# Optimization experiments

Measured on AMD Instinct MI355X. Metric: run time of the kernel, lower is better.

Reference implementation:

```python
import jax, jax.numpy as jnp
import numpy as np

BIG = 1e8   # fill value used by to_dense_batch for missing neighbors in the original
EPS_W = 1e-8
EPS_BN = 1e-5


def setup_inputs() -> dict:
    key = jax.random.key(0)
    ks = jax.random.split(key, 8)
    N, S, Dc, Df = 16384, 4096, 256, 64
    fine_xyz = jax.random.normal(ks[0], (1, 3, N), dtype=jnp.float32)
    coarse_xyz = jax.random.normal(ks[1], (1, 3, S), dtype=jnp.float32)
    fine_piece_id = jnp.sort(jax.random.randint(ks[2], (1, 1, N), 0, 4))
    coarse_piece_id = jnp.sort(jax.random.randint(ks[3], (1, 1, S), 0, 4))
    fine_features = jax.random.normal(ks[4], (1, Df, N), dtype=jnp.float32)
    coarse_features = jax.random.normal(ks[5], (1, Dc, S), dtype=jnp.float32)
    # mlp stack: Conv1d(320->256), Conv1d(256->128), each with BatchNorm1d
    W1 = jax.random.normal(ks[6], (256, Dc + Df), dtype=jnp.float32) * 0.05
    b1 = jnp.zeros((256,), jnp.float32)
    g1 = jnp.ones((256,), jnp.float32)
    be1 = jnp.zeros((256,), jnp.float32)
    W2 = jax.random.normal(ks[7], (128, 256), dtype=jnp.float32) * 0.05
    b2 = jnp.zeros((128,), jnp.float32)
    g2 = jnp.ones((128,), jnp.float32)
    be2 = jnp.zeros((128,), jnp.float32)
    return dict(fine_xyz=fine_xyz, coarse_xyz=coarse_xyz,
                fine_piece_id=fine_piece_id, coarse_piece_id=coarse_piece_id,
                fine_features=fine_features, coarse_features=coarse_features,
                W1=W1, b1=b1, g1=g1, be1=be1, W2=W2, b2=b2, g2=g2, be2=be2)


def _bn_relu(x, gamma, beta):
    # x: [N, C]; BatchNorm1d in training mode -> batch stats over the N axis
    mu = jnp.mean(x, axis=0, keepdims=True)
    var = jnp.mean((x - mu) ** 2, axis=0, keepdims=True)  # biased var, as torch BN
    return jax.nn.relu((x - mu) * jax.lax.rsqrt(var + EPS_BN) * gamma + beta)


def reference(fine_xyz, coarse_xyz, fine_piece_id, coarse_piece_id,
              fine_features, coarse_features, W1, b1, g1, be1, W2, b2, g2, be2):
    fxyz = fine_xyz[0].T            # [N, 3]
    cxyz = coarse_xyz[0].T          # [S, 3]
    ff = fine_features[0].T         # [N, Df]
    cf = coarse_features[0].T       # [S, Dc]
    fid = fine_piece_id.reshape(-1)     # [N]
    cid = coarse_piece_id.reshape(-1)   # [S]

    # squared euclidean distances, masked to the same piece (knn with batch vectors)
    d2 = (jnp.sum(fxyz ** 2, -1)[:, None] + jnp.sum(cxyz ** 2, -1)[None, :]
          - 2.0 * fxyz @ cxyz.T)                       # [N, S]
    d2 = jnp.where(fid[:, None] != cid[None, :], BIG, d2)

    neg_d, idx = jax.lax.top_k(-d2, 3)                  # 3-NN per fine point
    dist = -neg_d                                       # [N, 3]

    w = 1.0 / (dist + EPS_W)
    w = w / jnp.sum(w, axis=1, keepdims=True)           # [N, 3]

    gathered = cf[idx]                                  # [N, 3, Dc]
    interp = jnp.sum(gathered * w[:, :, None], axis=1)  # [N, Dc]

    x = jnp.concatenate([interp, ff], axis=-1)          # [N, Dc+Df]
    x = _bn_relu(x @ W1.T + b1, g1, be1)                # [N, 256]
    x = _bn_relu(x @ W2.T + b2, g2, be2)                # [N, 128]
    return x.T[None]                                    # [1, 128, N]
```

## Files before the change

kernel.cpp:

```cpp
#include <hip/hip_runtime.h>
#include <hip/hip_bf16.h>

#define N_FINE   16384
#define S_COARSE 4096
#define DC       256
#define DF       64
#define K1       320
#define C1       256
#define C2       128
#define BIGF     1e8f
#define EPS_W    1e-8f
#define EPS_BN   1e-5f
#define IMAX     0x7fffffff

typedef __attribute__((ext_vector_type(8))) short bf16x8;
typedef __attribute__((ext_vector_type(8))) unsigned short u16x8;
typedef __attribute__((ext_vector_type(4))) float f32x4;

#define OFF_CNT    128
#define OFF_RANGES 0
#define OFF_SUMS   256
#define OFF_SCALE1 3328
#define OFF_SHIFT1 4352
#define OFF_SCALE2 5376
#define OFF_SHIFT2 5888
#define OFF_CPACK  8192
#define OFF_CFT    73728
#define OFF_IDX3   4268032
#define OFF_W3     4464640
#define OFF_W1B    4661248
#define OFF_W2B    4825088
#define OFF_Y1     4890624
#define OFF_Y2     13279232

__device__ inline unsigned short f2bf_bits(float f) {
    __hip_bfloat16 h = __float2bfloat16(f);
    unsigned short u;
    __builtin_memcpy(&u, &h, 2);
    return u;
}

__global__ __launch_bounds__(256) void setup_kernel(
    const int* __restrict__ cid, int* __restrict__ ranges, float* __restrict__ sums,
    int* __restrict__ cnt,
    const float* __restrict__ cxyz, float4* __restrict__ cpack,
    const float* __restrict__ W1, const float* __restrict__ W2,
    unsigned short* __restrict__ W1b, unsigned short* __restrict__ W2b,
    const float* __restrict__ cf, float* __restrict__ cfT)
{
    __shared__ float tile[32][33];
    int b = blockIdx.x, t = threadIdx.x;
    if (b == 0) {
        if (t < 8) ranges[t] = 0;
        if (t < 2) cnt[t] = 0;
        for (int i = t; i < 768; i += 256) sums[i] = 0.f;
        __syncthreads();
        for (int s = t; s < S_COARSE; s += 256) {
            int c = cid[s];
            if (s == 0 || cid[s - 1] != c) ranges[c] = s;
            if (s == S_COARSE - 1 || cid[s + 1] != c) ranges[4 + c] = s + 1;
        }
    } else if (b <= 16) {
        int s = (b - 1) * 256 + t;
        float x = cxyz[s], y = cxyz[S_COARSE + s], z = cxyz[2 * S_COARSE + s];
        cpack[s] = make_float4(x, y, z, x * x + y * y + z * z);
    } else if (b <= 336) {
        int i = (b - 17) * 256 + t;
        W1b[i] = f2bf_bits(W1[i]);
        if (i < C2 * C1) W2b[i] = f2bf_bits(W2[i]);
    } else {
        int lb = b - 337;
        int tx = t & 31, ty = t >> 5;
        int s0 = (lb & 127) * 32, c0 = (lb >> 7) * 32;
        #pragma unroll
        for (int i = 0; i < 4; i++)
            tile[ty + i * 8][tx] = cf[(c0 + ty + i * 8) * S_COARSE + s0 + tx];
        __syncthreads();
        #pragma unroll
        for (int i = 0; i < 4; i++) {
            int s = ty + i * 8;
            cfT[(s0 + s) * DC + c0 + tx] = tile[tx][s];
        }
    }
}

__global__ __launch_bounds__(256) void knn_kernel(const float* __restrict__ fxyz,
                                                  const int* __restrict__ fpid,
                                                  const float4* __restrict__ cpack,
                                                  const int* __restrict__ ranges,
                                                  int* __restrict__ idx3,
                                                  float* __restrict__ w3) {
    int t = threadIdx.x;
    int lane = t & 63, wid = t >> 6;
    int n = blockIdx.x * 4 + wid;
    int fid = fpid[n];
    float fx = fxyz[n], fy = fxyz[N_FINE + n], fz = fxyz[2 * N_FINE + n];
    float fn2 = fx * fx + fy * fy + fz * fz;
    int st = ranges[fid], en = ranges[4 + fid];

    float d0 = BIGF, d1 = BIGF, d2v = BIGF;
    int i0 = IMAX, i1 = IMAX, i2 = IMAX;
    for (int s = st + lane; s < en; s += 64) {
        float4 c = cpack[s];
        float d = fn2 + c.w - 2.0f * (fx * c.x + fy * c.y + fz * c.z);
        if (d < d0)       { d2v = d1; i2 = i1; d1 = d0; i1 = i0; d0 = d; i0 = s; }
        else if (d < d1)  { d2v = d1; i2 = i1; d1 = d;  i1 = s; }
        else if (d < d2v) { d2v = d;  i2 = s; }
    }
    #pragma unroll
    for (int m = 1; m < 64; m <<= 1) {
        float e0 = __shfl_xor(d0, m, 64), e1 = __shfl_xor(d1, m, 64), e2 = __shfl_xor(d2v, m, 64);
        int   j0 = __shfl_xor(i0, m, 64), j1 = __shfl_xor(i1, m, 64), j2 = __shfl_xor(i2, m, 64);
        #pragma unroll
        for (int q = 0; q < 3; q++) {
            float e = (q == 0) ? e0 : (q == 1) ? e1 : e2;
            int   j = (q == 0) ? j0 : (q == 1) ? j1 : j2;
            bool b0 = (e < d0) || (e == d0 && j < i0);
            bool b1 = (e < d1) || (e == d1 && j < i1);
            bool b2 = (e < d2v) || (e == d2v && j < i2);
            if (b0)      { d2v = d1; i2 = i1; d1 = d0; i1 = i0; d0 = e; i0 = j; }
            else if (b1) { d2v = d1; i2 = i1; d1 = e;  i1 = j; }
            else if (b2) { d2v = e;  i2 = j; }
        }
    }
    if (lane == 0) {
        int cand = 0;
        while (i0 == IMAX || i1 == IMAX || i2 == IMAX) {
            if (cand >= st && cand < en) { cand = en; continue; }
            if (i0 == IMAX)      { i0 = cand; d0 = BIGF; }
            else if (i1 == IMAX) { i1 = cand; d1 = BIGF; }
            else                 { i2 = cand; d2v = BIGF; }
            cand++;
        }
        float w0 = 1.0f / (d0 + EPS_W);
        float w1 = 1.0f / (d1 + EPS_W);
        float w2 = 1.0f / (d2v + EPS_W);
        float inv = 1.0f / (w0 + w1 + w2);
        idx3[n * 3 + 0] = i0; idx3[n * 3 + 1] = i1; idx3[n * 3 + 2] = i2;
        w3[n * 3 + 0] = w0 * inv; w3[n * 3 + 1] = w1 * inv; w3[n * 3 + 2] = w2 * inv;
    }
}

__global__ __launch_bounds__(256) void gemm1_kernel(
    const int* __restrict__ idx3, const float* __restrict__ w3,
    const float* __restrict__ cfT, const float* __restrict__ ff,
    const unsigned short* __restrict__ W1b, const float* __restrict__ bias,
    unsigned short* __restrict__ Y1, float* __restrict__ sums, float* __restrict__ sumsq,
    const float* __restrict__ g, const float* __restrict__ be,
    float* __restrict__ scale, float* __restrict__ shift, int* __restrict__ cnt)
{
    __shared__ __align__(16) unsigned short As[4 * 32 * 8];
    __shared__ __align__(16) unsigned short Bs[4 * 256 * 8];
    __shared__ int   sI[32][3];
    __shared__ float sWt[32][3];
    __shared__ int isLast;
    int t = threadIdx.x;
    int m0 = blockIdx.x * 32;
    int lane = t & 63, wid = t >> 6;
    int wn = wid * 64;

    if (t < 32) {
        sI[t][0]  = idx3[(m0 + t) * 3 + 0];
        sI[t][1]  = idx3[(m0 + t) * 3 + 1];
        sI[t][2]  = idx3[(m0 + t) * 3 + 2];
        sWt[t][0] = w3[(m0 + t) * 3 + 0];
        sWt[t][1] = w3[(m0 + t) * 3 + 1];
        sWt[t][2] = w3[(m0 + t) * 3 + 2];
    }
    int ksA = t & 3, rowA = t >> 2;
    int fxw = ksA << 2;
    int gA = ksA * 32 + (rowA ^ fxw);
    int rowB = t;
    f32x4 acc[2][4] = {};
    int ks = lane >> 4, r16 = lane & 15, fxr = ks << 2;
    __syncthreads();

    for (int kt = 0; kt < K1; kt += 32) {
        u16x8 va;
        if (t < 128) {
            int k0 = kt + ksA * 8;
            if (k0 < DC) {
                int i0 = sI[rowA][0], i1 = sI[rowA][1], i2 = sI[rowA][2];
                float w0 = sWt[rowA][0], w1 = sWt[rowA][1], w2 = sWt[rowA][2];
                const float* c0p = &cfT[i0 * DC + k0];
                const float* c1p = &cfT[i1 * DC + k0];
                const float* c2p = &cfT[i2 * DC + k0];
                float4 a0 = *(const float4*)c0p, a1 = *(const float4*)(c0p + 4);
                float4 b0 = *(const float4*)c1p, b1 = *(const float4*)(c1p + 4);
                float4 e0 = *(const float4*)c2p, e1 = *(const float4*)(c2p + 4);
                va[0] = f2bf_bits(w0 * a0.x + w1 * b0.x + w2 * e0.x);
                va[1] = f2bf_bits(w0 * a0.y + w1 * b0.y + w2 * e0.y);
                va[2] = f2bf_bits(w0 * a0.z + w1 * b0.z + w2 * e0.z);
                va[3] = f2bf_bits(w0 * a0.w + w1 * b0.w + w2 * e0.w);
                va[4] = f2bf_bits(w0 * a1.x + w1 * b1.x + w2 * e1.x);
                va[5] = f2bf_bits(w0 * a1.y + w1 * b1.y + w2 * e1.y);
                va[6] = f2bf_bits(w0 * a1.z + w1 * b1.z + w2 * e1.z);
                va[7] = f2bf_bits(w0 * a1.w + w1 * b1.w + w2 * e1.w);
            } else {
                int c = k0 - DC;
                #pragma unroll
                for (int i = 0; i < 8; i++)
                    va[i] = f2bf_bits(ff[(c + i) * N_FINE + m0 + rowA]);
            }
        }
        u16x8 vb[4];
        #pragma unroll
        for (int kb = 0; kb < 4; kb++)
            vb[kb] = *(const u16x8*)&W1b[(size_t)rowB * K1 + kt + kb * 8];
        __syncthreads();
        if (t < 128) *(u16x8*)&As[gA * 8] = va;
        #pragma unroll
        for (int kb = 0; kb < 4; kb++)
            *(u16x8*)&Bs[(kb * 256 + (rowB ^ (kb << 2))) * 8] = vb[kb];
        __syncthreads();
        bf16x8 af[2], bfr[4];
        #pragma unroll
        for (int mi = 0; mi < 2; mi++)
            af[mi] = *(const bf16x8*)&As[(ks * 32 + ((mi * 16 + r16) ^ fxr)) * 8];
        #pragma unroll
        for (int nj = 0; nj < 4; nj++)
            bfr[nj] = *(const bf16x8*)&Bs[(ks * 256 + ((wn + nj * 16 + r16) ^ fxr)) * 8];
        #pragma unroll
        for (int mi = 0; mi < 2; mi++)
            #pragma unroll
            for (int nj = 0; nj < 4; nj++)
                acc[mi][nj] = __builtin_amdgcn_mfma_f32_16x16x32_bf16(af[mi], bfr[nj], acc[mi][nj], 0, 0, 0);
    }

    float sl[4] = {0.f, 0.f, 0.f, 0.f}, s2l[4] = {0.f, 0.f, 0.f, 0.f};
    #pragma unroll
    for (int nj = 0; nj < 4; nj++) {
        int n = wn + nj * 16 + r16;
        float bb = bias[n];
        #pragma unroll
        for (int mi = 0; mi < 2; mi++) {
            #pragma unroll
            for (int r = 0; r < 4; r++) {
                int m = m0 + mi * 16 + ks * 4 + r;
                float o = acc[mi][nj][r] + bb;
                Y1[(size_t)m * C1 + n] = f2bf_bits(o);
                sl[nj] += o; s2l[nj] += o * o;
            }
        }
    }
    #pragma unroll
    for (int nj = 0; nj < 4; nj++) {
        sl[nj]  += __shfl_xor(sl[nj],  16, 64);
        sl[nj]  += __shfl_xor(sl[nj],  32, 64);
        s2l[nj] += __shfl_xor(s2l[nj], 16, 64);
        s2l[nj] += __shfl_xor(s2l[nj], 32, 64);
    }
    if (lane < 16) {
        #pragma unroll
        for (int nj = 0; nj < 4; nj++) {
            atomicAdd(&sums[wn + nj * 16 + lane],  sl[nj]);
            atomicAdd(&sumsq[wn + nj * 16 + lane], s2l[nj]);
        }
    }
    __threadfence();
    __syncthreads();
    if (t == 0) isLast = (atomicAdd(cnt, 1) == (int)gridDim.x - 1);
    __syncthreads();
    if (isLast && t < C1) {
        float s  = atomicAdd(&sums[t], 0.f);
        float s2 = atomicAdd(&sumsq[t], 0.f);
        float mean = s * (1.0f / N_FINE);
        float var = s2 * (1.0f / N_FINE) - mean * mean;
        float sc = g[t] * rsqrtf(var + EPS_BN);
        scale[t] = sc;
        shift[t] = be[t] - mean * sc;
    }
}

template <int KDIM, int NOUT>
__global__ __launch_bounds__(256) void mfma_gemm2_kernel(
    const unsigned short* __restrict__ A,
    const unsigned short* __restrict__ B,
    const float* __restrict__ bias,
    const float* __restrict__ scale,
    const float* __restrict__ shift,
    float* __restrict__ Yout,
    float* __restrict__ sums, float* __restrict__ sumsq,
    const float* __restrict__ g, const float* __restrict__ be,
    float* __restrict__ scale2, float* __restrict__ shift2, int* __restrict__ cnt)
{
    __shared__ __align__(16) unsigned short As[4 * 128 * 8];
    __shared__ __align__(16) unsigned short Bs[4 * 64 * 8];
    __shared__ int isLast;
    int t = threadIdx.x;
    int m0 = blockIdx.x * 128, j0 = blockIdx.y * 64;
    int lane = t & 63, wid = t >> 6;
    int wm = (wid >> 1) * 64, wn = (wid & 1) * 32;

    int ksA = t & 3;
    int rowA0 = t >> 2;
    int rowA1 = 64 + rowA0;
    int fxw = ksA << 2;
    int gA0 = ksA * 128 + (rowA0 ^ fxw);
    int gA1 = ksA * 128 + (rowA1 ^ fxw);
    int gB  = ksA * 64 + (rowA0 ^ fxw);
    const unsigned short* pa0 = A + (size_t)(m0 + rowA0) * KDIM + ksA * 8;
    const unsigned short* pa1 = A + (size_t)(m0 + rowA1) * KDIM + ksA * 8;
    const unsigned short* pb  = B + (size_t)(j0 + rowA0) * KDIM + ksA * 8;

    f32x4 acc[4][2] = {};
    int ks = lane >> 4, r16 = lane & 15;
    int fxr = ks << 2;

    for (int kt = 0; kt < KDIM; kt += 32) {
        u16x8 va0 = *(const u16x8*)(pa0 + kt);
        u16x8 va1 = *(const u16x8*)(pa1 + kt);
        u16x8 vb  = *(const u16x8*)(pb + kt);
        int kb = kt + ksA * 8;
        #pragma unroll
        for (int i = 0; i < 8; i++) {
            float sc = scale[kb + i], sh = shift[kb + i];
            float f0 = __uint_as_float(((unsigned)va0[i]) << 16);
            float f1 = __uint_as_float(((unsigned)va1[i]) << 16);
            va0[i] = f2bf_bits(fmaxf(fmaf(f0, sc, sh), 0.f));
            va1[i] = f2bf_bits(fmaxf(fmaf(f1, sc, sh), 0.f));
        }
        __syncthreads();
        *(u16x8*)&As[gA0 * 8] = va0;
        *(u16x8*)&As[gA1 * 8] = va1;
        *(u16x8*)&Bs[gB * 8]  = vb;
        __syncthreads();
        bf16x8 af[4], bfr[2];
        #pragma unroll
        for (int mi = 0; mi < 4; mi++)
            af[mi] = *(const bf16x8*)&As[(ks * 128 + wm + mi * 16 + (r16 ^ fxr)) * 8];
        #pragma unroll
        for (int nj = 0; nj < 2; nj++)
            bfr[nj] = *(const bf16x8*)&Bs[(ks * 64 + wn + nj * 16 + (r16 ^ fxr)) * 8];
        #pragma unroll
        for (int mi = 0; mi < 4; mi++)
            #pragma unroll
            for (int nj = 0; nj < 2; nj++)
                acc[mi][nj] = __builtin_amdgcn_mfma_f32_16x16x32_bf16(af[mi], bfr[nj], acc[mi][nj], 0, 0, 0);
    }

    float sl[2] = {0.f, 0.f}, s2l[2] = {0.f, 0.f};
    #pragma unroll
    for (int nj = 0; nj < 2; nj++) {
        int n = j0 + wn + nj * 16 + r16;
        float bb = bias[n];
        #pragma unroll
        for (int mi = 0; mi < 4; mi++) {
            #pragma unroll
            for (int r = 0; r < 4; r++) {
                int m = m0 + wm + mi * 16 + ks * 4 + r;
                float o = acc[mi][nj][r] + bb;
                Yout[(size_t)m * NOUT + n] = o;
                sl[nj] += o; s2l[nj] += o * o;
            }
        }
    }
    #pragma unroll
    for (int nj = 0; nj < 2; nj++) {
        sl[nj]  += __shfl_xor(sl[nj],  16, 64);
        sl[nj]  += __shfl_xor(sl[nj],  32, 64);
        s2l[nj] += __shfl_xor(s2l[nj], 16, 64);
        s2l[nj] += __shfl_xor(s2l[nj], 32, 64);
    }
    if (lane < 16) {
        atomicAdd(&sums[j0 + wn + lane],       sl[0]);
        atomicAdd(&sums[j0 + wn + 16 + lane],  sl[1]);
        atomicAdd(&sumsq[j0 + wn + lane],      s2l[0]);
        atomicAdd(&sumsq[j0 + wn + 16 + lane], s2l[1]);
    }
    __threadfence();
    __syncthreads();
    if (t == 0) isLast = (atomicAdd(cnt, 1) == (int)(gridDim.x * gridDim.y) - 1);
    __syncthreads();
    if (isLast && t < NOUT) {
        float s  = atomicAdd(&sums[t], 0.f);
        float s2 = atomicAdd(&sumsq[t], 0.f);
        float mean = s * (1.0f / N_FINE);
        float var = s2 * (1.0f / N_FINE) - mean * mean;
        float sc = g[t] * rsqrtf(var + EPS_BN);
        scale2[t] = sc;
        shift2[t] = be[t] - mean * sc;
    }
}

__global__ __launch_bounds__(256) void out_kernel(const float* __restrict__ Y2,
                                                  const float* __restrict__ scale2,
                                                  const float* __restrict__ shift2,
                                                  float* __restrict__ out) {
    __shared__ float tile[64][65];
    int t = threadIdx.x;
    int n0 = blockIdx.x * 64, c0 = blockIdx.y * 64;
    int cl = t & 63, rg = t >> 6;
    #pragma unroll
    for (int i = 0; i < 16; i++) {
        int r = rg + i * 4;
        tile[r][cl] = Y2[(n0 + r) * C2 + c0 + cl];
    }
    __syncthreads();
    #pragma unroll
    for (int i = 0; i < 16; i++) {
        int c = rg + i * 4;
        float v = fmaf(tile[cl][c], scale2[c0 + c], shift2[c0 + c]);
        out[(c0 + c) * N_FINE + n0 + cl] = fmaxf(v, 0.f);
    }
}

extern "C" void kernel_launch(void* const* d_in, const int* in_sizes, int n_in,
                              void* d_out, int out_size, void* d_ws, size_t ws_size,
                              hipStream_t stream) {
    const float* fine_xyz   = (const float*)d_in[0];
    const float* coarse_xyz = (const float*)d_in[1];
    const int*   fine_pid   = (const int*)d_in[2];
    const int*   coarse_pid = (const int*)d_in[3];
    const float* fine_feat  = (const float*)d_in[4];
    const float* coarse_feat= (const float*)d_in[5];
    const float* W1  = (const float*)d_in[6];
    const float* b1  = (const float*)d_in[7];
    const float* g1  = (const float*)d_in[8];
    const float* be1 = (const float*)d_in[9];
    const float* W2  = (const float*)d_in[10];
    const float* b2  = (const float*)d_in[11];
    const float* g2  = (const float*)d_in[12];
    const float* be2 = (const float*)d_in[13];
    float* out = (float*)d_out;

    char* ws = (char*)d_ws;
    int*    ranges = (int*)(ws + OFF_RANGES);
    int*    cnt    = (int*)(ws + OFF_CNT);
    float*  sums1  = (float*)(ws + OFF_SUMS);
    float*  sumsq1 = sums1 + 256;
    float*  sums2  = sums1 + 512;
    float*  sumsq2 = sums1 + 640;
    float*  scale1 = (float*)(ws + OFF_SCALE1);
    float*  shift1 = (float*)(ws + OFF_SHIFT1);
    float*  scale2 = (float*)(ws + OFF_SCALE2);
    float*  shift2 = (float*)(ws + OFF_SHIFT2);
    float4* cpack  = (float4*)(ws + OFF_CPACK);
    float*  cfT    = (float*)(ws + OFF_CFT);
    int*    idx3   = (int*)(ws + OFF_IDX3);
    float*  w3     = (float*)(ws + OFF_W3);
    unsigned short* W1b = (unsigned short*)(ws + OFF_W1B);
    unsigned short* W2b = (unsigned short*)(ws + OFF_W2B);
    unsigned short* Y1  = (unsigned short*)(ws + OFF_Y1);
    float*          Y2  = (float*)(ws + OFF_Y2);

    setup_kernel<<<1361, 256, 0, stream>>>(coarse_pid, ranges, sums1, cnt,
                                           coarse_xyz, cpack, W1, W2, W1b, W2b,
                                           coarse_feat, cfT);
    knn_kernel<<<N_FINE / 4, 256, 0, stream>>>(fine_xyz, fine_pid, cpack, ranges, idx3, w3);

    gemm1_kernel<<<N_FINE / 32, 256, 0, stream>>>(idx3, w3, cfT, fine_feat,
                                                  W1b, b1, Y1, sums1, sumsq1,
                                                  g1, be1, scale1, shift1, cnt);

    mfma_gemm2_kernel<C1, C2><<<dim3(N_FINE / 128, C2 / 64), 256, 0, stream>>>(
        Y1, W2b, b2, scale1, shift1, Y2, sums2, sumsq2,
        g2, be2, scale2, shift2, cnt + 1);

    out_kernel<<<dim3(N_FINE / 64, C2 / 64), 256, 0, stream>>>(Y2, scale2, shift2, out);
}
```

Before: 224.3 us.

## Prefetch next K tile in GEMMs, shrink gemm2 tile, split BN finalize

Both GEMM kernels now load the next K-slice (gathered coarse features or fine features, W tiles, BN scale/shift) into registers while the current slice is computed, a register-level double buffer that hides global latency. gemm2 moves from 128x64 to 64x64 tiles to double the block count, and BN stats finalization moves from a last-block atomic counter into separate tiny finalize kernels, removing the threadfence and counter atomics. The cost is more register pressure, two extra kernel launches, and less reuse per gemm2 block.

```diff
diff --git a/kernel.cpp b/kernel.cpp
--- a/kernel.cpp
+++ b/kernel.cpp
@@ -17,7 +17,6 @@
 typedef __attribute__((ext_vector_type(8))) unsigned short u16x8;
 typedef __attribute__((ext_vector_type(4))) float f32x4;
 
-#define OFF_CNT    128
 #define OFF_RANGES 0
 #define OFF_SUMS   256
 #define OFF_SCALE1 3328
@@ -39,10 +38,12 @@
     __builtin_memcpy(&u, &h, 2);
     return u;
 }
+__device__ inline float bf2f(unsigned short u) {
+    return __uint_as_float(((unsigned)u) << 16);
+}
 
 __global__ __launch_bounds__(256) void setup_kernel(
     const int* __restrict__ cid, int* __restrict__ ranges, float* __restrict__ sums,
-    int* __restrict__ cnt,
     const float* __restrict__ cxyz, float4* __restrict__ cpack,
     const float* __restrict__ W1, const float* __restrict__ W2,
     unsigned short* __restrict__ W1b, unsigned short* __restrict__ W2b,
@@ -52,7 +53,6 @@
     int b = blockIdx.x, t = threadIdx.x;
     if (b == 0) {
         if (t < 8) ranges[t] = 0;
-        if (t < 2) cnt[t] = 0;
         for (int i = t; i < 768; i += 256) sums[i] = 0.f;
         __syncthreads();
         for (int s = t; s < S_COARSE; s += 256) {
@@ -145,15 +145,12 @@
     const int* __restrict__ idx3, const float* __restrict__ w3,
     const float* __restrict__ cfT, const float* __restrict__ ff,
     const unsigned short* __restrict__ W1b, const float* __restrict__ bias,
-    unsigned short* __restrict__ Y1, float* __restrict__ sums, float* __restrict__ sumsq,
-    const float* __restrict__ g, const float* __restrict__ be,
-    float* __restrict__ scale, float* __restrict__ shift, int* __restrict__ cnt)
+    unsigned short* __restrict__ Y1, float* __restrict__ sums, float* __restrict__ sumsq)
 {
     __shared__ __align__(16) unsigned short As[4 * 32 * 8];
     __shared__ __align__(16) unsigned short Bs[4 * 256 * 8];
     __shared__ int   sI[32][3];
     __shared__ float sWt[32][3];
-    __shared__ int isLast;
     int t = threadIdx.x;
     int m0 = blockIdx.x * 32;
     int lane = t & 63, wid = t >> 6;
@@ -175,38 +172,71 @@
     int ks = lane >> 4, r16 = lane & 15, fxr = ks << 2;
     __syncthreads();
 
+    const float *c0p = nullptr, *c1p = nullptr, *c2p = nullptr;
+    float w0v = 0.f, w1v = 0.f, w2v = 0.f;
+    if (t < 128) {
+        c0p = &cfT[sI[rowA][0] * DC];
+        c1p = &cfT[sI[rowA][1] * DC];
+        c2p = &cfT[sI[rowA][2] * DC];
+        w0v = sWt[rowA][0]; w1v = sWt[rowA][1]; w2v = sWt[rowA][2];
+    }
+    const unsigned short* pb = &W1b[(size_t)rowB * K1];
+
+    float r[24];
+    u16x8 vb[4];
+
+    {
+        int k0 = ksA * 8;
+        if (t < 128) {
+            *(float4*)&r[0]  = *(const float4*)(c0p + k0);
+            *(float4*)&r[4]  = *(const float4*)(c0p + k0 + 4);
+            *(float4*)&r[8]  = *(const float4*)(c1p + k0);
+            *(float4*)&r[12] = *(const float4*)(c1p + k0 + 4);
+            *(float4*)&r[16] = *(const float4*)(c2p + k0);
+            *(float4*)&r[20] = *(const float4*)(c2p + k0 + 4);
+        }
+        #pragma unroll
+        for (int kb = 0; kb < 4; kb++) vb[kb] = *(const u16x8*)(pb + kb * 8);
+    }
+
+    #pragma unroll
     for (int kt = 0; kt < K1; kt += 32) {
         u16x8 va;
         if (t < 128) {
             int k0 = kt + ksA * 8;
             if (k0 < DC) {
-                int i0 = sI[rowA][0], i1 = sI[rowA][1], i2 = sI[rowA][2];
-                float w0 = sWt[rowA][0], w1 = sWt[rowA][1], w2 = sWt[rowA][2];
-                const float* c0p = &cfT[i0 * DC + k0];
-                const float* c1p = &cfT[i1 * DC + k0];
-                const float* c2p = &cfT[i2 * DC + k0];
-                float4 a0 = *(const float4*)c0p, a1 = *(const float4*)(c0p + 4);
-                float4 b0 = *(const float4*)c1p, b1 = *(const float4*)(c1p + 4);
-                float4 e0 = *(const float4*)c2p, e1 = *(const float4*)(c2p + 4);
-                va[0] = f2bf_bits(w0 * a0.x + w1 * b0.x + w2 * e0.x);
-                va[1] = f2bf_bits(w0 * a0.y + w1 * b0.y + w2 * e0.y);
-                va[2] = f2bf_bits(w0 * a0.z + w1 * b0.z + w2 * e0.z);
-                va[3] = f2bf_bits(w0 * a0.w + w1 * b0.w + w2 * e0.w);
-                va[4] = f2bf_bits(w0 * a1.x + w1 * b1.x + w2 * e1.x);
-                va[5] = f2bf_bits(w0 * a1.y + w1 * b1.y + w2 * e1.y);
-                va[6] = f2bf_bits(w0 * a1.z + w1 * b1.z + w2 * e1.z);
-                va[7] = f2bf_bits(w0 * a1.w + w1 * b1.w + w2 * e1.w);
-            } else {
-                int c = k0 - DC;
                 #pragma unroll
                 for (int i = 0; i < 8; i++)
-                    va[i] = f2bf_bits(ff[(c + i) * N_FINE + m0 + rowA]);
+                    va[i] = f2bf_bits(w0v * r[i] + w1v * r[8 + i] + w2v * r[16 + i]);
+            } else {
+                #pragma unroll
+                for (int i = 0; i < 8; i++)
+                    va[i] = f2bf_bits(r[i]);
             }
         }
-        u16x8 vb[4];
-        #pragma unroll
-        for (int kb = 0; kb < 4; kb++)
-            vb[kb] = *(const u16x8*)&W1b[(size_t)rowB * K1 + kt + kb * 8];
+        float rn[24];
+        u16x8 vbn[4];
+        if (kt + 32 < K1) {
+            int k0n = kt + 32 + ksA * 8;
+            if (t < 128) {
+                if (k0n < DC) {
+                    *(float4*)&rn[0]  = *(const float4*)(c0p + k0n);
+                    *(float4*)&rn[4]  = *(const float4*)(c0p + k0n + 4);
+                    *(float4*)&rn[8]  = *(const float4*)(c1p + k0n);
+                    *(float4*)&rn[12] = *(const float4*)(c1p + k0n + 4);
+                    *(float4*)&rn[16] = *(const float4*)(c2p + k0n);
+                    *(float4*)&rn[20] = *(const float4*)(c2p + k0n + 4);
+                } else {
+                    int c = k0n - DC;
+                    #pragma unroll
+                    for (int i = 0; i < 8; i++)
+                        rn[i] = ff[(size_t)(c + i) * N_FINE + m0 + rowA];
+                }
+            }
+            #pragma unroll
+            for (int kb = 0; kb < 4; kb++)
+                vbn[kb] = *(const u16x8*)(pb + kt + 32 + kb * 8);
+        }
         __syncthreads();
         if (t < 128) *(u16x8*)&As[gA * 8] = va;
         #pragma unroll
@@ -225,6 +255,12 @@
             #pragma unroll
             for (int nj = 0; nj < 4; nj++)
                 acc[mi][nj] = __builtin_amdgcn_mfma_f32_16x16x32_bf16(af[mi], bfr[nj], acc[mi][nj], 0, 0, 0);
+        if (kt + 32 < K1) {
+            #pragma unroll
+            for (int i = 0; i < 24; i++) r[i] = rn[i];
+            #pragma unroll
+            for (int kb = 0; kb < 4; kb++) vb[kb] = vbn[kb];
+        }
     }
 
     float sl[4] = {0.f, 0.f, 0.f, 0.f}, s2l[4] = {0.f, 0.f, 0.f, 0.f};
@@ -235,9 +271,9 @@
         #pragma unroll
         for (int mi = 0; mi < 2; mi++) {
             #pragma unroll
-            for (int r = 0; r < 4; r++) {
-                int m = m0 + mi * 16 + ks * 4 + r;
-                float o = acc[mi][nj][r] + bb;
+            for (int r4 = 0; r4 < 4; r4++) {
+                int m = m0 + mi * 16 + ks * 4 + r4;
+                float o = acc[mi][nj][r4] + bb;
                 Y1[(size_t)m * C1 + n] = f2bf_bits(o);
                 sl[nj] += o; s2l[nj] += o * o;
             }
@@ -256,19 +292,6 @@
             atomicAdd(&sums[wn + nj * 16 + lane],  sl[nj]);
             atomicAdd(&sumsq[wn + nj * 16 + lane], s2l[nj]);
         }
-    }
-    __threadfence();
-    __syncthreads();
-    if (t == 0) isLast = (atomicAdd(cnt, 1) == (int)gridDim.x - 1);
-    __syncthreads();
-    if (isLast && t < C1) {
-        float s  = atomicAdd(&sums[t], 0.f);
-        float s2 = atomicAdd(&sumsq[t], 0.f);
-        float mean = s * (1.0f / N_FINE);
-        float var = s2 * (1.0f / N_FINE) - mean * mean;
-        float sc = g[t] * rsqrtf(var + EPS_BN);
-        scale[t] = sc;
-        shift[t] = be[t] - mean * sc;
     }
 }
 
@@ -280,63 +303,76 @@
     const float* __restrict__ scale,
     const float* __restrict__ shift,
     float* __restrict__ Yout,
-    float* __restrict__ sums, float* __restrict__ sumsq,
-    const float* __restrict__ g, const float* __restrict__ be,
-    float* __restrict__ scale2, float* __restrict__ shift2, int* __restrict__ cnt)
+    float* __restrict__ sums, float* __restrict__ sumsq)
 {
-    __shared__ __align__(16) unsigned short As[4 * 128 * 8];
+    __shared__ __align__(16) unsigned short As[4 * 64 * 8];
     __shared__ __align__(16) unsigned short Bs[4 * 64 * 8];
-    __shared__ int isLast;
     int t = threadIdx.x;
-    int m0 = blockIdx.x * 128, j0 = blockIdx.y * 64;
+    int m0 = blockIdx.x * 64, j0 = blockIdx.y * 64;
     int lane = t & 63, wid = t >> 6;
-    int wm = (wid >> 1) * 64, wn = (wid & 1) * 32;
+    int wm = (wid >> 1) * 32, wn = (wid & 1) * 32;
 
     int ksA = t & 3;
-    int rowA0 = t >> 2;
-    int rowA1 = 64 + rowA0;
+    int rowA = t >> 2;
     int fxw = ksA << 2;
-    int gA0 = ksA * 128 + (rowA0 ^ fxw);
-    int gA1 = ksA * 128 + (rowA1 ^ fxw);
-    int gB  = ksA * 64 + (rowA0 ^ fxw);
-    const unsigned short* pa0 = A + (size_t)(m0 + rowA0) * KDIM + ksA * 8;
-    const unsigned short* pa1 = A + (size_t)(m0 + rowA1) * KDIM + ksA * 8;
-    const unsigned short* pb  = B + (size_t)(j0 + rowA0) * KDIM + ksA * 8;
-
-    f32x4 acc[4][2] = {};
+    int gA = ksA * 64 + (rowA ^ fxw);
+    const unsigned short* pa = A + (size_t)(m0 + rowA) * KDIM + ksA * 8;
+    const unsigned short* pb = B + (size_t)(j0 + rowA) * KDIM + ksA * 8;
+
+    f32x4 acc[2][2] = {};
     int ks = lane >> 4, r16 = lane & 15;
     int fxr = ks << 2;
 
+    u16x8 va, vb;
+    float4 sc0, sc1, sh0, sh1;
+    va = *(const u16x8*)pa;
+    vb = *(const u16x8*)pb;
+    sc0 = *(const float4*)&scale[ksA * 8];
+    sc1 = *(const float4*)&scale[ksA * 8 + 4];
+    sh0 = *(const float4*)&shift[ksA * 8];
+    sh1 = *(const float4*)&shift[ksA * 8 + 4];
+
+    #pragma unroll
     for (int kt = 0; kt < KDIM; kt += 32) {
-        u16x8 va0 = *(const u16x8*)(pa0 + kt);
-        u16x8 va1 = *(const u16x8*)(pa1 + kt);
-        u16x8 vb  = *(const u16x8*)(pb + kt);
-        int kb = kt + ksA * 8;
-        #pragma unroll
-        for (int i = 0; i < 8; i++) {
-            float sc = scale[kb + i], sh = shift[kb + i];
-            float f0 = __uint_as_float(((unsigned)va0[i]) << 16);
-            float f1 = __uint_as_float(((unsigned)va1[i]) << 16);
-            va0[i] = f2bf_bits(fmaxf(fmaf(f0, sc, sh), 0.f));
-            va1[i] = f2bf_bits(fmaxf(fmaf(f1, sc, sh), 0.f));
-        }
-        __syncthreads();
-        *(u16x8*)&As[gA0 * 8] = va0;
-        *(u16x8*)&As[gA1 * 8] = va1;
-        *(u16x8*)&Bs[gB * 8]  = vb;
-        __syncthreads();
-        bf16x8 af[4], bfr[2];
-        #pragma unroll
-        for (int mi = 0; mi < 4; mi++)
-            af[mi] = *(const bf16x8*)&As[(ks * 128 + wm + mi * 16 + (r16 ^ fxr)) * 8];
+        u16x8 vat;
+        {
+            float scv[8] = {sc0.x, sc0.y, sc0.z, sc0.w, sc1.x, sc1.y, sc1.z, sc1.w};
+            float shv[8] = {sh0.x, sh0.y, sh0.z, sh0.w, sh1.x, sh1.y, sh1.z, sh1.w};
+            #pragma unroll
+            for (int i = 0; i < 8; i++)
+                vat[i] = f2bf_bits(fmaxf(fmaf(bf2f(va[i]), scv[i], shv[i]), 0.f));
+        }
+        u16x8 van, vbn;
+        float4 sc0n, sc1n, sh0n, sh1n;
+        if (kt + 32 < KDIM) {
+            van = *(const u16x8*)(pa + kt + 32);
+            vbn = *(const u16x8*)(pb + kt + 32);
+            int kb = kt + 32 + ksA * 8;
+            sc0n = *(const float4*)&scale[kb];
+            sc1n = *(const float4*)&scale[kb + 4];
+            sh0n = *(const float4*)&shift[kb];
+            sh1n = *(const float4*)&shift[kb + 4];
+        }
+        __syncthreads();
+        *(u16x8*)&As[gA * 8] = vat;
+        *(u16x8*)&Bs[gA * 8] = vb;
+        __syncthreads();
+        bf16x8 af[2], bfr[2];
+        #pragma unroll
+        for (int mi = 0; mi < 2; mi++)
+            af[mi] = *(const bf16x8*)&As[(ks * 64 + ((wm + mi * 16 + r16) ^ fxr)) * 8];
         #pragma unroll
         for (int nj = 0; nj < 2; nj++)
-            bfr[nj] = *(const bf16x8*)&Bs[(ks * 64 + wn + nj * 16 + (r16 ^ fxr)) * 8];
-        #pragma unroll
-        for (int mi = 0; mi < 4; mi++)
+            bfr[nj] = *(const bf16x8*)&Bs[(ks * 64 + ((wn + nj * 16 + r16) ^ fxr)) * 8];
+        #pragma unroll
+        for (int mi = 0; mi < 2; mi++)
             #pragma unroll
             for (int nj = 0; nj < 2; nj++)
                 acc[mi][nj] = __builtin_amdgcn_mfma_f32_16x16x32_bf16(af[mi], bfr[nj], acc[mi][nj], 0, 0, 0);
+        if (kt + 32 < KDIM) {
+            va = van; vb = vbn;
+            sc0 = sc0n; sc1 = sc1n; sh0 = sh0n; sh1 = sh1n;
+        }
     }
 
     float sl[2] = {0.f, 0.f}, s2l[2] = {0.f, 0.f};
@@ -345,11 +381,11 @@
         int n = j0 + wn + nj * 16 + r16;
         float bb = bias[n];
         #pragma unroll
-        for (int mi = 0; mi < 4; mi++) {
-            #pragma unroll
-            for (int r = 0; r < 4; r++) {
-                int m = m0 + wm + mi * 16 + ks * 4 + r;
-                float o = acc[mi][nj][r] + bb;
+        for (int mi = 0; mi < 2; mi++) {
+            #pragma unroll
+            for (int r4 = 0; r4 < 4; r4++) {
+                int m = m0 + wm + mi * 16 + ks * 4 + r4;
+                float o = acc[mi][nj][r4] + bb;
                 Yout[(size_t)m * NOUT + n] = o;
                 sl[nj] += o; s2l[nj] += o * o;
             }
@@ -368,18 +404,18 @@
         atomicAdd(&sumsq[j0 + wn + lane],      s2l[0]);
         atomicAdd(&sumsq[j0 + wn + 16 + lane], s2l[1]);
     }
-    __threadfence();
-    __syncthreads();
-    if (t == 0) isLast = (atomicAdd(cnt, 1) == (int)(gridDim.x * gridDim.y) - 1);
-    __syncthreads();
-    if (isLast && t < NOUT) {
-        float s  = atomicAdd(&sums[t], 0.f);
-        float s2 = atomicAdd(&sumsq[t], 0.f);
-        float mean = s * (1.0f / N_FINE);
-        float var = s2 * (1.0f / N_FINE) - mean * mean;
+}
+
+__global__ void finalize_kernel(const float* __restrict__ sums, const float* __restrict__ sumsq,
+                                const float* __restrict__ g, const float* __restrict__ be,
+                                float* __restrict__ scale, float* __restrict__ shift, int C) {
+    int t = threadIdx.x;
+    if (t < C) {
+        float mean = sums[t] * (1.0f / N_FINE);
+        float var = sumsq[t] * (1.0f / N_FINE) - mean * mean;
         float sc = g[t] * rsqrtf(var + EPS_BN);
-        scale2[t] = sc;
-        shift2[t] = be[t] - mean * sc;
+        scale[t] = sc;
+        shift[t] = be[t] - mean * sc;
     }
 }
 
@@ -426,7 +462,6 @@
 
     char* ws = (char*)d_ws;
     int*    ranges = (int*)(ws + OFF_RANGES);
-    int*    cnt    = (int*)(ws + OFF_CNT);
     float*  sums1  = (float*)(ws + OFF_SUMS);
     float*  sumsq1 = sums1 + 256;
     float*  sums2  = sums1 + 512;
@@ -444,18 +479,18 @@
     unsigned short* Y1  = (unsigned short*)(ws + OFF_Y1);
     float*          Y2  = (float*)(ws + OFF_Y2);
 
-    setup_kernel<<<1361, 256, 0, stream>>>(coarse_pid, ranges, sums1, cnt,
+    setup_kernel<<<1361, 256, 0, stream>>>(coarse_pid, ranges, sums1,
                                            coarse_xyz, cpack, W1, W2, W1b, W2b,
                                            coarse_feat, cfT);
     knn_kernel<<<N_FINE / 4, 256, 0, stream>>>(fine_xyz, fine_pid, cpack, ranges, idx3, w3);
 
     gemm1_kernel<<<N_FINE / 32, 256, 0, stream>>>(idx3, w3, cfT, fine_feat,
-                                                  W1b, b1, Y1, sums1, sumsq1,
-                                                  g1, be1, scale1, shift1, cnt);
-
-    mfma_gemm2_kernel<C1, C2><<<dim3(N_FINE / 128, C2 / 64), 256, 0, stream>>>(
-        Y1, W2b, b2, scale1, shift1, Y2, sums2, sumsq2,
-        g2, be2, scale2, shift2, cnt + 1);
+                                                  W1b, b1, Y1, sums1, sumsq1);
+    finalize_kernel<<<1, 256, 0, stream>>>(sums1, sumsq1, g1, be1, scale1, shift1, C1);
+
+    mfma_gemm2_kernel<C1, C2><<<dim3(N_FINE / 64, C2 / 64), 256, 0, stream>>>(
+        Y1, W2b, b2, scale1, shift1, Y2, sums2, sumsq2);
+    finalize_kernel<<<1, 256, 0, stream>>>(sums2, sumsq2, g2, be2, scale2, shift2, C2);
 
     out_kernel<<<dim3(N_FINE / 64, C2 / 64), 256, 0, stream>>>(Y2, scale2, shift2, out);
 }
```

Result: faster. 180.6 us (-19.5%).
